# Performance work log

Measured on AMD Instinct MI355X. Metric: run time of the kernel, lower is better.

Reference implementation:

```python
import jax, jax.numpy as jnp
import numpy as np

N_NODES = 50000
N_EDGES = 800000
IN_CH = 128
OUT_CH = 64
HID_CH = 2 * OUT_CH  # 128


def gcn_conv(x, edge_index, W, b, n_nodes):
    """PyG GCNConv: linear -> add self-loops -> sym-normalized scatter-add -> bias."""
    h = x @ W  # [N, out]
    loop = jnp.arange(n_nodes)
    row = jnp.concatenate([edge_index[0], loop])  # source nodes
    col = jnp.concatenate([edge_index[1], loop])  # target nodes
    deg = jax.ops.segment_sum(jnp.ones_like(col, dtype=h.dtype), col, num_segments=n_nodes)
    dinv = jnp.where(deg > 0, jax.lax.rsqrt(jnp.maximum(deg, 1.0)), 0.0)
    norm = dinv[row] * dinv[col]  # [E+N]
    msg = h[row] * norm[:, None]  # gather + scale, [E+N, out]
    out = jax.ops.segment_sum(msg, col, num_segments=n_nodes)  # scatter-add
    return out + b


def setup_inputs() -> dict:
    key = jax.random.key(0)
    ks = jax.random.split(key, 9)
    x = jax.random.normal(ks[0], (N_NODES, IN_CH), dtype=jnp.float32)
    edge_index = jax.random.randint(ks[1], (2, N_EDGES), 0, N_NODES, dtype=jnp.int64)
    s_in = 1.0 / np.sqrt(IN_CH)
    s_hid = 1.0 / np.sqrt(HID_CH)
    W1 = jax.random.normal(ks[2], (IN_CH, HID_CH), dtype=jnp.float32) * s_in
    b1 = jnp.zeros((HID_CH,), dtype=jnp.float32)
    W2 = jax.random.normal(ks[3], (HID_CH, OUT_CH), dtype=jnp.float32) * s_hid
    b2 = jnp.zeros((OUT_CH,), dtype=jnp.float32)
    W3 = jax.random.normal(ks[4], (HID_CH, OUT_CH), dtype=jnp.float32) * s_hid
    b3 = jnp.zeros((OUT_CH,), dtype=jnp.float32)
    return {"x": x, "edge_index": edge_index, "W1": W1, "b1": b1,
            "W2": W2, "b2": b2, "W3": W3, "b3": b3}


def reference(x, edge_index, W1, b1, W2, b2, W3, b3):
    act = jax.nn.relu
    hidden = act(gcn_conv(x, edge_index, W1, b1, N_NODES))
    x1 = act(gcn_conv(hidden, edge_index, W2, b2, N_NODES))
    x2 = act(gcn_conv(hidden, edge_index, W3, b3, N_NODES))
    return (x1, x2)
```

## Files before the change

kernel.cpp:

```cpp
#include <hip/hip_runtime.h>

#define N_NODES 50000
#define N_EDGES 800000
#define CH 128
#define SCAN_BLKS 98
#define WT_PAD 136

typedef __attribute__((ext_vector_type(8))) short short8;
typedef __attribute__((ext_vector_type(4))) float floatx4;

__device__ __forceinline__ short f2bf(float f) {
    union { float f; unsigned u; } v; v.f = f;
    unsigned r = v.u + 0x7fff + ((v.u >> 16) & 1);
    return (short)(r >> 16);
}
__device__ __forceinline__ float bflo(unsigned u) {
    union { unsigned u; float f; } v; v.u = u << 16; return v.f;
}
__device__ __forceinline__ float bfhi(unsigned u) {
    union { unsigned u; float f; } v; v.u = u & 0xffff0000u; return v.f;
}


__global__ void rank_kernel(const int* __restrict__ ei, int* __restrict__ counts,
                            int* __restrict__ rank) {
    int e = blockIdx.x * blockDim.x + threadIdx.x;
    if (e < N_EDGES) rank[e] = atomicAdd(&counts[ei[N_EDGES + e]], 1);
}

__global__ __launch_bounds__(256) void scan_block_kernel(const int* __restrict__ counts,
                                                         int* __restrict__ row_ptr,
                                                         float* __restrict__ dinv,
                                                         int* __restrict__ bsum) {
    __shared__ int s[256];
    int tid = threadIdx.x;
    int base = blockIdx.x * 512;
    int i0 = base + 2 * tid, i1 = i0 + 1;
    int v0 = (i0 < N_NODES) ? counts[i0] : 0;
    int v1 = (i1 < N_NODES) ? counts[i1] : 0;
    if (i0 < N_NODES) dinv[i0] = rsqrtf((float)(v0 + 1));
    if (i1 < N_NODES) dinv[i1] = rsqrtf((float)(v1 + 1));
    int t = v0 + v1;
    s[tid] = t;
    __syncthreads();
    for (int off = 1; off < 256; off <<= 1) {
        int tmp = (tid >= off) ? s[tid - off] : 0;
        __syncthreads();
        s[tid] += tmp;
        __syncthreads();
    }
    int pre = s[tid] - t;
    if (i0 < N_NODES) row_ptr[i0] = pre;
    if (i1 < N_NODES) row_ptr[i1] = pre + v0;
    if (tid == 255) bsum[blockIdx.x] = s[255];
}

__global__ __launch_bounds__(128) void scan_tops_kernel(const int* __restrict__ bsum,
                                                        int* __restrict__ boff,
                                                        int* __restrict__ row_ptr) {
    __shared__ int s[128];
    int tid = threadIdx.x;
    int v = (tid < SCAN_BLKS) ? bsum[tid] : 0;
    s[tid] = v;
    __syncthreads();
    for (int off = 1; off < 128; off <<= 1) {
        int tmp = (tid >= off) ? s[tid - off] : 0;
        __syncthreads();
        s[tid] += tmp;
        __syncthreads();
    }
    if (tid < SCAN_BLKS) boff[tid] = s[tid] - v;
    if (tid == 127) row_ptr[N_NODES] = s[127];
}

__global__ __launch_bounds__(256) void scan_add_kernel(int* __restrict__ row_ptr,
                                                       const int* __restrict__ boff) {
    int base = blockIdx.x * 512;
    int off = boff[blockIdx.x];
    for (int i = base + threadIdx.x; i < base + 512; i += 256)
        if (i < N_NODES) row_ptr[i] += off;
}

__global__ void scatter_plain(const int* __restrict__ ei, const int* __restrict__ row_ptr,
                              const int* __restrict__ rank, int* __restrict__ sorted_src) {
    int e = blockIdx.x * blockDim.x + threadIdx.x;
    if (e < N_EDGES) {
        int dst = ei[N_EDGES + e];
        sorted_src[row_ptr[dst] + rank[e]] = ei[e];
    }
}


__global__ void prep_weights(const float* __restrict__ W1, const float* __restrict__ W2,
                             const float* __restrict__ W3, const float* __restrict__ b2,
                             const float* __restrict__ b3, unsigned short* __restrict__ Wt1,
                             unsigned short* __restrict__ Wt23, float* __restrict__ b23) {
    int i = blockIdx.x * blockDim.x + threadIdx.x;
    if (i < 128 * 128) {
        int n = i >> 7, k = i & 127;
        Wt1[i] = (unsigned short)f2bf(W1[k * 128 + n]);
        float w = (n < 64) ? W2[k * 64 + n] : W3[k * 64 + (n - 64)];
        Wt23[i] = (unsigned short)f2bf(w);
    } else if (i < 128 * 128 + 128) {
        int k2 = i - 128 * 128;
        b23[k2] = (k2 < 64) ? b2[k2] : b3[k2 - 64];
    }
}


template <bool A_BF16>
__global__ __launch_bounds__(256) void gemm_mfma(const void* __restrict__ Ain,
                                                 const unsigned short* __restrict__ Wt,
                                                 const float* __restrict__ dinv,
                                                 unsigned short* __restrict__ g) {
    __shared__ unsigned short lds[128 * WT_PAD];
    int tid = threadIdx.x;
    int wave = tid >> 6, lane = tid & 63;
    int quad = lane >> 4, ln = lane & 15;

    {
        int r = tid >> 1, h = tid & 1;
        const int4* src = (const int4*)(Wt + r * 128 + h * 64);
#pragma unroll
        for (int i = 0; i < 8; ++i)
            *(int4*)&lds[r * WT_PAD + h * 64 + i * 8] = src[i];
    }

    int row_base = blockIdx.x * 64 + wave * 16;
    int arow = row_base + ln;
    bool ok = arow < N_NODES;
    short8 afrag[4];
    if (A_BF16) {
        const unsigned short* A = (const unsigned short*)Ain;
#pragma unroll
        for (int kk = 0; kk < 4; ++kk) {
            short8 v = {};
            if (ok) v = *(const short8*)(A + arow * 128 + kk * 32 + quad * 8);
            afrag[kk] = v;
        }
    } else {
        const float* A = (const float*)Ain;
#pragma unroll
        for (int kk = 0; kk < 4; ++kk) {
            short8 v = {};
            if (ok) {
                const float* p = A + arow * 128 + kk * 32 + quad * 8;
#pragma unroll
                for (int j = 0; j < 8; ++j) v[j] = f2bf(p[j]);
            }
            afrag[kk] = v;
        }
    }
    __syncthreads();

    floatx4 acc[8] = {};
#pragma unroll
    for (int n0 = 0; n0 < 8; ++n0) {
#pragma unroll
        for (int kk = 0; kk < 4; ++kk) {
            short8 b = *(const short8*)&lds[(n0 * 16 + ln) * WT_PAD + kk * 32 + quad * 8];
            acc[n0] = __builtin_amdgcn_mfma_f32_16x16x32_bf16(afrag[kk], b, acc[n0], 0, 0, 0);
        }
    }

    __syncthreads();
    unsigned short* st = &lds[wave * 16 * WT_PAD];
    float dv[4];
#pragma unroll
    for (int r = 0; r < 4; ++r) {
        int node = row_base + quad * 4 + r;
        dv[r] = (node < N_NODES) ? dinv[node] : 0.f;
    }
#pragma unroll
    for (int n0 = 0; n0 < 8; ++n0)
#pragma unroll
        for (int r = 0; r < 4; ++r)
            st[(quad * 4 + r) * WT_PAD + n0 * 16 + ln] =
                (unsigned short)f2bf(acc[n0][r] * dv[r]);
    __syncthreads();

#pragma unroll
    for (int i = 0; i < 4; ++i) {
        int row = i * 4 + quad;
        int node = row_base + row;
        short8 v = *(const short8*)&st[row * WT_PAD + ln * 8];
        if (node < N_NODES) *(short8*)(g + node * 128 + ln * 8) = v;
    }
}


template <int MODE>
__global__ __launch_bounds__(256) void aggregate_bf16(const unsigned short* __restrict__ g,
                                                      const float* __restrict__ dinv,
                                                      const int* __restrict__ row_ptr,
                                                      const int* __restrict__ srcs,
                                                      const float* __restrict__ bias,
                                                      void* __restrict__ outp) {
    int sub = threadIdx.x >> 5;
    int n = blockIdx.x * 8 + sub;
    if (n >= N_NODES) return;
    int c2 = threadIdx.x & 31;
    const uint2* grow = (const uint2*)g;
    uint2 u = grow[n * 32 + c2];
    float a0 = bflo(u.x), a1 = bfhi(u.x), a2 = bflo(u.y), a3 = bfhi(u.y);
    float b0 = 0.f, b1 = 0.f, b2_ = 0.f, b3_ = 0.f;
    int e = row_ptr[n], end = row_ptr[n + 1];
    for (; e + 3 < end; e += 4) {
        int s0 = srcs[e], s1 = srcs[e + 1], s2 = srcs[e + 2], s3 = srcs[e + 3];
        uint2 v0 = grow[s0 * 32 + c2];
        uint2 v1 = grow[s1 * 32 + c2];
        uint2 v2 = grow[s2 * 32 + c2];
        uint2 v3 = grow[s3 * 32 + c2];
        a0 += bflo(v0.x); a1 += bfhi(v0.x); a2 += bflo(v0.y); a3 += bfhi(v0.y);
        b0 += bflo(v1.x); b1 += bfhi(v1.x); b2_ += bflo(v1.y); b3_ += bfhi(v1.y);
        a0 += bflo(v2.x); a1 += bfhi(v2.x); a2 += bflo(v2.y); a3 += bfhi(v2.y);
        b0 += bflo(v3.x); b1 += bfhi(v3.x); b2_ += bflo(v3.y); b3_ += bfhi(v3.y);
    }
    for (; e < end; ++e) {
        uint2 v = grow[srcs[e] * 32 + c2];
        a0 += bflo(v.x); a1 += bfhi(v.x); a2 += bflo(v.y); a3 += bfhi(v.y);
    }
    a0 += b0; a1 += b1; a2 += b2_; a3 += b3_;
    float d = dinv[n];
    float4 bv = ((const float4*)bias)[c2];
    float o0 = fmaxf(d * a0 + bv.x, 0.f);
    float o1 = fmaxf(d * a1 + bv.y, 0.f);
    float o2 = fmaxf(d * a2 + bv.z, 0.f);
    float o3 = fmaxf(d * a3 + bv.w, 0.f);
    if (MODE == 0) {
        unsigned short* h = (unsigned short*)outp;
        uint2 w;
        w.x = ((unsigned)(unsigned short)f2bf(o0)) | (((unsigned)(unsigned short)f2bf(o1)) << 16);
        w.y = ((unsigned)(unsigned short)f2bf(o2)) | (((unsigned)(unsigned short)f2bf(o3)) << 16);
        ((uint2*)h)[n * 32 + c2] = w;
    } else {
        float* out = (float*)outp;
        float4 o = make_float4(o0, o1, o2, o3);
        if (c2 < 16) ((float4*)out)[n * 16 + c2] = o;
        else ((float4*)(out + N_NODES * 64))[n * 16 + (c2 - 16)] = o;
    }
}


extern "C" void kernel_launch(void* const* d_in, const int* in_sizes, int n_in,
                              void* d_out, int out_size, void* d_ws, size_t ws_size,
                              hipStream_t stream) {
    const float* x  = (const float*)d_in[0];
    const int*   ei = (const int*)d_in[1];
    const float* W1 = (const float*)d_in[2];
    const float* b1 = (const float*)d_in[3];
    const float* W2 = (const float*)d_in[4];
    const float* b2 = (const float*)d_in[5];
    const float* W3 = (const float*)d_in[6];
    const float* b3 = (const float*)d_in[7];
    float* out = (float*)d_out;

    char* w = (char*)d_ws;
    int*            counts     = (int*)(w + 0);
    int*            row_ptr    = (int*)(w + 204800);
    float*          dinv       = (float*)(w + 409600);
    int*            rank       = (int*)(w + 614400);
    int*            sorted_src = (int*)(w + 3814400);
    unsigned short* Wt1        = (unsigned short*)(w + 7014400);
    unsigned short* Wt23       = (unsigned short*)(w + 7047168);
    float*          b23        = (float*)(w + 7079936);
    int*            bsum       = (int*)(w + 7080448);
    int*            boff       = (int*)(w + 7080960);
    unsigned short* g1         = (unsigned short*)(w + 8388608);
    unsigned short* hidden     = (unsigned short*)(w + 25165824);

    hipMemsetAsync(counts, 0, N_NODES * sizeof(int), stream);
    prep_weights<<<65, 256, 0, stream>>>(W1, W2, W3, b2, b3, Wt1, Wt23, b23);
    rank_kernel<<<(N_EDGES + 255) / 256, 256, 0, stream>>>(ei, counts, rank);
    scan_block_kernel<<<SCAN_BLKS, 256, 0, stream>>>(counts, row_ptr, dinv, bsum);
    scan_tops_kernel<<<1, 128, 0, stream>>>(bsum, boff, row_ptr);
    scan_add_kernel<<<SCAN_BLKS, 256, 0, stream>>>(row_ptr, boff);
    scatter_plain<<<(N_EDGES + 255) / 256, 256, 0, stream>>>(ei, row_ptr, rank, sorted_src);

    const int gemm_blocks = (N_NODES + 63) / 64;
    const int agg_blocks = (N_NODES + 7) / 8;

    gemm_mfma<false><<<gemm_blocks, 256, 0, stream>>>(x, Wt1, dinv, g1);
    aggregate_bf16<0><<<agg_blocks, 256, 0, stream>>>(g1, dinv, row_ptr, sorted_src, b1, hidden);

    gemm_mfma<true><<<gemm_blocks, 256, 0, stream>>>(hidden, Wt23, dinv, g1);
    aggregate_bf16<1><<<agg_blocks, 256, 0, stream>>>(g1, dinv, row_ptr, sorted_src, b23, out);
}
```

Before: 236.8 us.

## Pad CSR rows to multiples of four with dummy zero node, vectorize index loads

Each node's CSR segment is padded to a multiple of 4, and padding slots point to a dummy zero row placed just past g1. This lets the aggregation loop load indices as int4 and unroll by 8 with no scalar tail. The counts memset is folded into the weight-prep kernel, and the two top-level scan kernels are merged into one that also fills the padding. In exchange it makes extra gathers from the dummy row and grows sorted_src.

```diff
diff --git a/kernel.cpp b/kernel.cpp
--- a/kernel.cpp
+++ b/kernel.cpp
@@ -5,6 +5,7 @@
 #define CH 128
 #define SCAN_BLKS 98
 #define WT_PAD 136
+#define DUMMY N_NODES
 
 typedef __attribute__((ext_vector_type(8))) short short8;
 typedef __attribute__((ext_vector_type(4))) float floatx4;
@@ -19,6 +20,32 @@
 }
 __device__ __forceinline__ float bfhi(unsigned u) {
     union { unsigned u; float f; } v; v.u = u & 0xffff0000u; return v.f;
+}
+
+
+__global__ __launch_bounds__(256) void prep_kernel(const float* __restrict__ W1,
+                                                   const float* __restrict__ W2,
+                                                   const float* __restrict__ W3,
+                                                   const float* __restrict__ b2,
+                                                   const float* __restrict__ b3,
+                                                   unsigned short* __restrict__ Wt1,
+                                                   unsigned short* __restrict__ Wt23,
+                                                   float* __restrict__ b23,
+                                                   int* __restrict__ counts,
+                                                   unsigned int* __restrict__ gdummy) {
+    int i = blockIdx.x * blockDim.x + threadIdx.x;
+    if (i < 128 * 128) {
+        int n = i >> 7, k = i & 127;
+        Wt1[i] = (unsigned short)f2bf(W1[k * 128 + n]);
+        float w = (n < 64) ? W2[k * 64 + n] : W3[k * 64 + (n - 64)];
+        Wt23[i] = (unsigned short)f2bf(w);
+    } else if (i < 128 * 128 + 128) {
+        int k2 = i - 128 * 128;
+        b23[k2] = (k2 < 64) ? b2[k2] : b3[k2 - 64];
+    } else if (i < 128 * 128 + 192) {
+        gdummy[i - (128 * 128 + 128)] = 0;
+    }
+    for (int j = i; j < N_NODES; j += 66 * 256) counts[j] = 0;
 }
 
 
@@ -40,7 +67,8 @@
     int v1 = (i1 < N_NODES) ? counts[i1] : 0;
     if (i0 < N_NODES) dinv[i0] = rsqrtf((float)(v0 + 1));
     if (i1 < N_NODES) dinv[i1] = rsqrtf((float)(v1 + 1));
-    int t = v0 + v1;
+    int p0 = (v0 + 3) & ~3, p1 = (v1 + 3) & ~3;
+    int t = p0 + p1;
     s[tid] = t;
     __syncthreads();
     for (int off = 1; off < 256; off <<= 1) {
@@ -51,34 +79,35 @@
     }
     int pre = s[tid] - t;
     if (i0 < N_NODES) row_ptr[i0] = pre;
-    if (i1 < N_NODES) row_ptr[i1] = pre + v0;
+    if (i1 < N_NODES) row_ptr[i1] = pre + p0;
     if (tid == 255) bsum[blockIdx.x] = s[255];
 }
 
-__global__ __launch_bounds__(128) void scan_tops_kernel(const int* __restrict__ bsum,
-                                                        int* __restrict__ boff,
-                                                        int* __restrict__ row_ptr) {
+__global__ __launch_bounds__(256) void scan_fix_kernel(int* __restrict__ row_ptr,
+                                                       const int* __restrict__ bsum,
+                                                       const int* __restrict__ degs,
+                                                       int* __restrict__ sorted_src) {
     __shared__ int s[128];
     int tid = threadIdx.x;
-    int v = (tid < SCAN_BLKS) ? bsum[tid] : 0;
-    s[tid] = v;
+    if (tid < 128) s[tid] = (tid < SCAN_BLKS) ? bsum[tid] : 0;
     __syncthreads();
     for (int off = 1; off < 128; off <<= 1) {
-        int tmp = (tid >= off) ? s[tid - off] : 0;
+        int t = (tid < 128 && tid >= off) ? s[tid - off] : 0;
         __syncthreads();
-        s[tid] += tmp;
+        if (tid < 128) s[tid] += t;
         __syncthreads();
     }
-    if (tid < SCAN_BLKS) boff[tid] = s[tid] - v;
-    if (tid == 127) row_ptr[N_NODES] = s[127];
-}
-
-__global__ __launch_bounds__(256) void scan_add_kernel(int* __restrict__ row_ptr,
-                                                       const int* __restrict__ boff) {
+    int blockoff = (blockIdx.x == 0) ? 0 : s[blockIdx.x - 1];
     int base = blockIdx.x * 512;
-    int off = boff[blockIdx.x];
-    for (int i = base + threadIdx.x; i < base + 512; i += 256)
-        if (i < N_NODES) row_ptr[i] += off;
+    for (int i = base + tid; i < base + 512; i += 256) {
+        if (i < N_NODES) {
+            int v = row_ptr[i] + blockoff;
+            row_ptr[i] = v;
+            int d = degs[i];
+            int pc = (d + 3) & ~3;
+            for (int p = v + d; p < v + pc; ++p) sorted_src[p] = DUMMY;
+        }
+    }
 }
 
 __global__ void scatter_plain(const int* __restrict__ ei, const int* __restrict__ row_ptr,
@@ -87,23 +116,6 @@
     if (e < N_EDGES) {
         int dst = ei[N_EDGES + e];
         sorted_src[row_ptr[dst] + rank[e]] = ei[e];
-    }
-}
-
-
-__global__ void prep_weights(const float* __restrict__ W1, const float* __restrict__ W2,
-                             const float* __restrict__ W3, const float* __restrict__ b2,
-                             const float* __restrict__ b3, unsigned short* __restrict__ Wt1,
-                             unsigned short* __restrict__ Wt23, float* __restrict__ b23) {
-    int i = blockIdx.x * blockDim.x + threadIdx.x;
-    if (i < 128 * 128) {
-        int n = i >> 7, k = i & 127;
-        Wt1[i] = (unsigned short)f2bf(W1[k * 128 + n]);
-        float w = (n < 64) ? W2[k * 64 + n] : W3[k * 64 + (n - 64)];
-        Wt23[i] = (unsigned short)f2bf(w);
-    } else if (i < 128 * 128 + 128) {
-        int k2 = i - 128 * 128;
-        b23[k2] = (k2 < 64) ? b2[k2] : b3[k2 - 64];
     }
 }
 
@@ -193,6 +205,7 @@
 __global__ __launch_bounds__(256) void aggregate_bf16(const unsigned short* __restrict__ g,
                                                       const float* __restrict__ dinv,
                                                       const int* __restrict__ row_ptr,
+                                                      const int* __restrict__ degs,
                                                       const int* __restrict__ srcs,
                                                       const float* __restrict__ bias,
                                                       void* __restrict__ outp) {
@@ -204,21 +217,39 @@
     uint2 u = grow[n * 32 + c2];
     float a0 = bflo(u.x), a1 = bfhi(u.x), a2 = bflo(u.y), a3 = bfhi(u.y);
     float b0 = 0.f, b1 = 0.f, b2_ = 0.f, b3_ = 0.f;
-    int e = row_ptr[n], end = row_ptr[n + 1];
-    for (; e + 3 < end; e += 4) {
-        int s0 = srcs[e], s1 = srcs[e + 1], s2 = srcs[e + 2], s3 = srcs[e + 3];
-        uint2 v0 = grow[s0 * 32 + c2];
-        uint2 v1 = grow[s1 * 32 + c2];
-        uint2 v2 = grow[s2 * 32 + c2];
-        uint2 v3 = grow[s3 * 32 + c2];
+    int beg = row_ptr[n];
+    int pend = beg + ((degs[n] + 3) & ~3);
+    int e = beg;
+    for (; e + 8 <= pend; e += 8) {
+        int4 sa = *(const int4*)&srcs[e];
+        int4 sb = *(const int4*)&srcs[e + 4];
+        uint2 v0 = grow[sa.x * 32 + c2];
+        uint2 v1 = grow[sa.y * 32 + c2];
+        uint2 v2 = grow[sa.z * 32 + c2];
+        uint2 v3 = grow[sa.w * 32 + c2];
+        uint2 v4 = grow[sb.x * 32 + c2];
+        uint2 v5 = grow[sb.y * 32 + c2];
+        uint2 v6 = grow[sb.z * 32 + c2];
+        uint2 v7 = grow[sb.w * 32 + c2];
         a0 += bflo(v0.x); a1 += bfhi(v0.x); a2 += bflo(v0.y); a3 += bfhi(v0.y);
         b0 += bflo(v1.x); b1 += bfhi(v1.x); b2_ += bflo(v1.y); b3_ += bfhi(v1.y);
         a0 += bflo(v2.x); a1 += bfhi(v2.x); a2 += bflo(v2.y); a3 += bfhi(v2.y);
         b0 += bflo(v3.x); b1 += bfhi(v3.x); b2_ += bflo(v3.y); b3_ += bfhi(v3.y);
-    }
-    for (; e < end; ++e) {
-        uint2 v = grow[srcs[e] * 32 + c2];
-        a0 += bflo(v.x); a1 += bfhi(v.x); a2 += bflo(v.y); a3 += bfhi(v.y);
+        a0 += bflo(v4.x); a1 += bfhi(v4.x); a2 += bflo(v4.y); a3 += bfhi(v4.y);
+        b0 += bflo(v5.x); b1 += bfhi(v5.x); b2_ += bflo(v5.y); b3_ += bfhi(v5.y);
+        a0 += bflo(v6.x); a1 += bfhi(v6.x); a2 += bflo(v6.y); a3 += bfhi(v6.y);
+        b0 += bflo(v7.x); b1 += bfhi(v7.x); b2_ += bflo(v7.y); b3_ += bfhi(v7.y);
+    }
+    if (e < pend) {
+        int4 sa = *(const int4*)&srcs[e];
+        uint2 v0 = grow[sa.x * 32 + c2];
+        uint2 v1 = grow[sa.y * 32 + c2];
+        uint2 v2 = grow[sa.z * 32 + c2];
+        uint2 v3 = grow[sa.w * 32 + c2];
+        a0 += bflo(v0.x); a1 += bfhi(v0.x); a2 += bflo(v0.y); a3 += bfhi(v0.y);
+        b0 += bflo(v1.x); b1 += bfhi(v1.x); b2_ += bflo(v1.y); b3_ += bfhi(v1.y);
+        a0 += bflo(v2.x); a1 += bfhi(v2.x); a2 += bflo(v2.y); a3 += bfhi(v2.y);
+        b0 += bflo(v3.x); b1 += bfhi(v3.x); b2_ += bflo(v3.y); b3_ += bfhi(v3.y);
     }
     a0 += b0; a1 += b1; a2 += b2_; a3 += b3_;
     float d = dinv[n];
@@ -261,28 +292,26 @@
     float*          dinv       = (float*)(w + 409600);
     int*            rank       = (int*)(w + 614400);
     int*            sorted_src = (int*)(w + 3814400);
-    unsigned short* Wt1        = (unsigned short*)(w + 7014400);
-    unsigned short* Wt23       = (unsigned short*)(w + 7047168);
-    float*          b23        = (float*)(w + 7079936);
-    int*            bsum       = (int*)(w + 7080448);
-    int*            boff       = (int*)(w + 7080960);
+    unsigned short* Wt1        = (unsigned short*)(w + 7614400);
+    unsigned short* Wt23       = (unsigned short*)(w + 7647168);
+    float*          b23        = (float*)(w + 7679936);
+    int*            bsum       = (int*)(w + 7680448);
     unsigned short* g1         = (unsigned short*)(w + 8388608);
-    unsigned short* hidden     = (unsigned short*)(w + 25165824);
-
-    hipMemsetAsync(counts, 0, N_NODES * sizeof(int), stream);
-    prep_weights<<<65, 256, 0, stream>>>(W1, W2, W3, b2, b3, Wt1, Wt23, b23);
+    unsigned short* hidden     = (unsigned short*)(w + 22020096);
+
+    prep_kernel<<<66, 256, 0, stream>>>(W1, W2, W3, b2, b3, Wt1, Wt23, b23, counts,
+                                        (unsigned int*)(g1 + N_NODES * 128));
     rank_kernel<<<(N_EDGES + 255) / 256, 256, 0, stream>>>(ei, counts, rank);
     scan_block_kernel<<<SCAN_BLKS, 256, 0, stream>>>(counts, row_ptr, dinv, bsum);
-    scan_tops_kernel<<<1, 128, 0, stream>>>(bsum, boff, row_ptr);
-    scan_add_kernel<<<SCAN_BLKS, 256, 0, stream>>>(row_ptr, boff);
+    scan_fix_kernel<<<SCAN_BLKS, 256, 0, stream>>>(row_ptr, bsum, counts, sorted_src);
     scatter_plain<<<(N_EDGES + 255) / 256, 256, 0, stream>>>(ei, row_ptr, rank, sorted_src);
 
     const int gemm_blocks = (N_NODES + 63) / 64;
     const int agg_blocks = (N_NODES + 7) / 8;
 
     gemm_mfma<false><<<gemm_blocks, 256, 0, stream>>>(x, Wt1, dinv, g1);
-    aggregate_bf16<0><<<agg_blocks, 256, 0, stream>>>(g1, dinv, row_ptr, sorted_src, b1, hidden);
+    aggregate_bf16<0><<<agg_blocks, 256, 0, stream>>>(g1, dinv, row_ptr, counts, sorted_src, b1, hidden);
 
     gemm_mfma<true><<<gemm_blocks, 256, 0, stream>>>(hidden, Wt23, dinv, g1);
-    aggregate_bf16<1><<<agg_blocks, 256, 0, stream>>>(g1, dinv, row_ptr, sorted_src, b23, out);
-}
+    aggregate_bf16<1><<<agg_blocks, 256, 0, stream>>>(g1, dinv, row_ptr, counts, sorted_src, b23, out);
+}
```

Result: faster. 225.9 us (-4.6%).
